# Kernel optimization log

Measured on AMD Instinct MI355X. Metric: run time of the kernel, lower is better.

Reference implementation:

```python
import jax, jax.numpy as jnp
import numpy as np

B, NQ, NKV = 2, 1024, 4096
DQ = 1024          # query_dim == context_dim
H, DH = 16, 64     # heads, dim_head
INNER = H * DH     # 1024
SCALE = DH ** -0.5


def setup_inputs() -> dict:
    key = jax.random.key(0)
    ks = jax.random.split(key, 6)
    s = 1.0 / np.sqrt(DQ)
    return {
        "x": jax.random.normal(ks[0], (B, NQ, DQ), dtype=jnp.float32),
        "context": jax.random.normal(ks[1], (B, NKV, DQ), dtype=jnp.float32),
        "Wq": jax.random.normal(ks[2], (DQ, INNER), dtype=jnp.float32) * s,
        "Wkv": jax.random.normal(ks[3], (DQ, 2 * INNER), dtype=jnp.float32) * s,
        "Wout": jax.random.normal(ks[4], (INNER, DQ), dtype=jnp.float32) * (1.0 / np.sqrt(INNER)),
        "b_out": jax.random.normal(ks[5], (DQ,), dtype=jnp.float32) * 0.01,
    }


def _split_heads(t):
    # b n (h d) -> b h n d
    b, n, _ = t.shape
    return t.reshape(b, n, H, DH).transpose(0, 2, 1, 3)


def reference(x, context, Wq, Wkv, Wout, b_out):
    q = x @ Wq                       # [B, NQ, INNER]
    kv = context @ Wkv               # [B, NKV, 2*INNER]
    k, v = jnp.split(kv, 2, axis=-1)
    q, k, v = map(_split_heads, (q, k, v))          # [B, H, n, DH]
    sim = jnp.einsum("bhid,bhjd->bhij", q, k) * SCALE  # [B, H, NQ, NKV]
    attn = jax.nn.softmax(sim, axis=-1)
    out = jnp.einsum("bhij,bhjd->bhid", attn, v)       # [B, H, NQ, DH]
    out = out.transpose(0, 2, 1, 3).reshape(B, NQ, INNER)  # (b h) n d -> b n (h d)
    return out @ Wout + b_out
```

## Files before the change

### kernel.cpp

```cpp
#include <hip/hip_runtime.h>
#include <stdint.h>

#define B_    2
#define NQ_   1024
#define NKV_  4096
#define DQ_   1024
#define H_    16
#define DH_   64
#define INNER_ 1024

typedef unsigned short u16;
typedef uint32_t u32;
typedef __bf16 bf16x8 __attribute__((ext_vector_type(8)));
typedef float  f32x4  __attribute__((ext_vector_type(4)));

__device__ __forceinline__ u16 f2bf(float x) {
  union { float f; uint32_t u; } v; v.f = x;
  uint32_t r = v.u + 0x7FFFu + ((v.u >> 16) & 1u);
  return (u16)(r >> 16);
}
__device__ __forceinline__ u32 pack2(float a, float b) {
  return (u32)f2bf(a) | ((u32)f2bf(b) << 16);
}
__device__ __forceinline__ u32 pack2rn(float a, float b) {
  union { float f; u32 u; } x, y; x.f = a; y.f = b;
  return __builtin_amdgcn_perm(y.u + 0x8000u, x.u + 0x8000u, 0x07060302u);
}
__device__ __forceinline__ float bf2f(u16 s) {
  union { float f; uint32_t u; } v; v.u = ((uint32_t)s) << 16; return v.f;
}

__device__ __forceinline__ void gload16(const void* g, void* l) {
  __builtin_amdgcn_global_load_lds((const __attribute__((address_space(1))) void*)g,
                                   (__attribute__((address_space(3))) void*)l,
                                   16, 0, 0);
}

__global__ __launch_bounds__(256) void prep(const float* __restrict__ x,
                                            const float* __restrict__ ctx,
                                            const float* __restrict__ Wq,
                                            const float* __restrict__ Wkv,
                                            const float* __restrict__ Wout,
                                            u16* __restrict__ xb,
                                            u16* __restrict__ ctxb,
                                            u16* __restrict__ WqT,
                                            u16* __restrict__ WkvT,
                                            u16* __restrict__ WoutT) {
  int bid = blockIdx.x;
  if (bid < 10240) {
    const float* src; u16* dst; int blk;
    if (bid < 2048) { src = x; dst = xb; blk = bid; }
    else            { src = ctx; dst = ctxb; blk = bid - 2048; }
    int i = (blk * 256 + threadIdx.x) * 4;
    float4 v = *(const float4*)(src + i);
    uint2 o; o.x = pack2(v.x, v.y); o.y = pack2(v.z, v.w);
    *(uint2*)(dst + i) = o;
    return;
  }
  __shared__ float tile[32][33];
  const float* W; u16* Wt; int K, N, local, nsh;
  if (bid < 11264)      { W = Wq;   Wt = WqT;   K = 1024; N = 1024; local = bid - 10240; nsh = 5; }
  else if (bid < 13312) { W = Wkv;  Wt = WkvT;  K = 1024; N = 2048; local = bid - 11264; nsh = 6; }
  else                  { W = Wout; Wt = WoutT; K = 1024; N = 1024; local = bid - 13312; nsh = 5; }
  int n0 = (local & ((1 << nsh) - 1)) * 32;
  int k0 = (local >> nsh) * 32;
  int tx = threadIdx.x & 31, ty = threadIdx.x >> 5;
  for (int i = ty; i < 32; i += 8)
    tile[i][tx] = W[(size_t)(k0 + i) * N + n0 + tx];
  __syncthreads();
  for (int i = ty; i < 32; i += 8)
    Wt[(size_t)(n0 + i) * K + k0 + tx] = f2bf(tile[tx][i]);
}

__global__ __launch_bounds__(256) void qkv_gemm(const u16* __restrict__ xb,
                                                const u16* __restrict__ ctxb,
                                                const u16* __restrict__ WqT,
                                                const u16* __restrict__ WkvT,
                                                u16* __restrict__ qb,
                                                u16* __restrict__ kb,
                                                u16* __restrict__ vTb) {
  __shared__ __align__(16) u16 As[128 * 32];
  __shared__ __align__(16) u16 Bs[128 * 32];
  const int tid = threadIdx.x;
  const int lane = tid & 63;
  const int w = tid >> 6;
  const int wr = w >> 1, wc = w & 1;
  const int l15 = lane & 15, quad = lane >> 4;

  int bid = blockIdx.x;
  const u16 *A, *Bt; int m0, n0, mode;
  if (bid < 128) { m0 = (bid >> 3) * 128; n0 = (bid & 7) * 128; A = xb;   Bt = WqT;  mode = 0; }
  else { bid -= 128; m0 = (bid >> 4) * 128; n0 = (bid & 15) * 128; A = ctxb; Bt = WkvT;
         mode = (n0 < 1024) ? 1 : 2; }
  const int K = 1024;

  const u16* Ab = A + (size_t)m0 * K;
  const u16* Bb = Bt + (size_t)n0 * K;

  f32x4 acc[4][4] = {};

  const int q1 = w * 64 + lane;
  const int q2 = q1 + 256;
  const int ar1 = q1 >> 2, ac1 = (q1 & 3) << 3;
  const int ar2 = q2 >> 2, ac2 = (q2 & 3) << 3;

  for (int k0 = 0; k0 < K; k0 += 32) {
    __syncthreads();
    gload16(Ab + (size_t)ar1 * K + k0 + ac1, &As[w * 512]);
    gload16(Ab + (size_t)ar2 * K + k0 + ac2, &As[2048 + w * 512]);
    gload16(Bb + (size_t)ar1 * K + k0 + ac1, &Bs[w * 512]);
    gload16(Bb + (size_t)ar2 * K + k0 + ac2, &Bs[2048 + w * 512]);
    __syncthreads();
    bf16x8 af[4], bfr[4];
#pragma unroll
    for (int i = 0; i < 4; ++i)
      af[i] = *(const bf16x8*)&As[(wr * 64 + i * 16 + l15) * 32 + quad * 8];
#pragma unroll
    for (int j = 0; j < 4; ++j)
      bfr[j] = *(const bf16x8*)&Bs[(wc * 64 + j * 16 + l15) * 32 + quad * 8];
#pragma unroll
    for (int i = 0; i < 4; ++i)
#pragma unroll
      for (int j = 0; j < 4; ++j)
        acc[i][j] = __builtin_amdgcn_mfma_f32_16x16x32_bf16(af[i], bfr[j], acc[i][j], 0, 0, 0);
  }

  if (mode == 2) {
    const int bb = m0 >> 12;
#pragma unroll
    for (int i = 0; i < 4; ++i) {
      int kvr = (m0 & 4095) + wr * 64 + i * 16 + quad * 4;
#pragma unroll
      for (int j = 0; j < 4; ++j) {
        int c = (n0 - 1024) + wc * 64 + j * 16 + l15;
        int h = c >> 6, dh = c & 63;
        uint2 st;
        st.x = pack2(acc[i][j][0], acc[i][j][1]);
        st.y = pack2(acc[i][j][2], acc[i][j][3]);
        *(uint2*)&vTb[((size_t)((bb * 16 + h) * 64 + dh)) * NKV_ + kvr] = st;
      }
    }
    return;
  }

  u16* out = (mode == 0) ? qb : kb;
  const int N = 1024;
#pragma unroll
  for (int i = 0; i < 4; ++i)
#pragma unroll
    for (int j = 0; j < 4; ++j) {
      int col = n0 + wc * 64 + j * 16 + l15;
#pragma unroll
      for (int r = 0; r < 4; ++r) {
        int row = m0 + wr * 64 + i * 16 + quad * 4 + r;
        out[(size_t)row * N + col] = f2bf(acc[i][j][r]);
      }
    }
}

__global__ __launch_bounds__(256) void out_gemm(const u16* __restrict__ A,
                                                const u16* __restrict__ Bt,
                                                float* __restrict__ Cout,
                                                const float* __restrict__ bias) {
  __shared__ __align__(16) u16 As[128 * 32];
  __shared__ __align__(16) u16 Bs[128 * 32];
  const int tid = threadIdx.x;
  const int lane = tid & 63;
  const int w = tid >> 6;
  const int wr = w >> 1, wc = w & 1;
  const int l15 = lane & 15, quad = lane >> 4;
  const int m0 = blockIdx.y * 128, n0 = blockIdx.x * 128;
  const int K = 1024, N = 1024;

  const u16* Ab = A + (size_t)m0 * K;
  const u16* Bb = Bt + (size_t)n0 * K;
  f32x4 acc[4][4] = {};

  const int q1 = w * 64 + lane, q2 = q1 + 256;
  const int ar1 = q1 >> 2, ac1 = (q1 & 3) << 3;
  const int ar2 = q2 >> 2, ac2 = (q2 & 3) << 3;

  for (int k0 = 0; k0 < K; k0 += 32) {
    __syncthreads();
    gload16(Ab + (size_t)ar1 * K + k0 + ac1, &As[w * 512]);
    gload16(Ab + (size_t)ar2 * K + k0 + ac2, &As[2048 + w * 512]);
    gload16(Bb + (size_t)ar1 * K + k0 + ac1, &Bs[w * 512]);
    gload16(Bb + (size_t)ar2 * K + k0 + ac2, &Bs[2048 + w * 512]);
    __syncthreads();
    bf16x8 af[4], bfr[4];
#pragma unroll
    for (int i = 0; i < 4; ++i)
      af[i] = *(const bf16x8*)&As[(wr * 64 + i * 16 + l15) * 32 + quad * 8];
#pragma unroll
    for (int j = 0; j < 4; ++j)
      bfr[j] = *(const bf16x8*)&Bs[(wc * 64 + j * 16 + l15) * 32 + quad * 8];
#pragma unroll
    for (int i = 0; i < 4; ++i)
#pragma unroll
      for (int j = 0; j < 4; ++j)
        acc[i][j] = __builtin_amdgcn_mfma_f32_16x16x32_bf16(af[i], bfr[j], acc[i][j], 0, 0, 0);
  }

#pragma unroll
  for (int i = 0; i < 4; ++i)
#pragma unroll
    for (int j = 0; j < 4; ++j) {
      int col = n0 + wc * 64 + j * 16 + l15;
      float bv = bias[col];
#pragma unroll
      for (int r = 0; r < 4; ++r) {
        int row = m0 + wr * 64 + i * 16 + quad * 4 + r;
        Cout[(size_t)row * N + col] = acc[i][j][r] + bv;
      }
    }
}

__global__ __launch_bounds__(256, 2) void attn_kernel(const u16* __restrict__ qg,
                                                      const u16* __restrict__ kb,
                                                      const u16* __restrict__ vT,
                                                      u16* __restrict__ attn_out) {
  __shared__ __align__(16) u16 Ks[128 * 64];
  __shared__ __align__(16) u16 Vs[64 * 128];
  __shared__ __align__(16) u32 P32[4 * 4 * 16 * 20];
  __shared__ float Lr[4][4][16];

  const int tid = threadIdx.x;
  const int lane = tid & 63;
  const int w = tid >> 6;
  const int l15 = lane & 15, quad = lane >> 4;
  const int bh = blockIdx.x, b = bh >> 4, h = bh & 15;
  const int q0 = blockIdx.y * 64;

  const float SC = 0.125f * 1.44269504088896340736f;
  union { u16 s[8]; bf16x8 v; } qf[4][2];
#pragma unroll
  for (int t = 0; t < 4; ++t)
#pragma unroll
    for (int kc = 0; kc < 2; ++kc) {
      const u16* qp = qg + (size_t)(b * NQ_ + q0 + t * 16 + l15) * INNER_ + h * 64 +
                      kc * 32 + quad * 8;
      union { u16 s[8]; uint4 u; } tmp;
      tmp.u = *(const uint4*)qp;
#pragma unroll
      for (int e = 0; e < 8; ++e) qf[t][kc].s[e] = f2bf(bf2f(tmp.s[e]) * SC);
    }

  f32x4 Oacc[4][4] = {};
  float l_lane[4] = {0.f, 0.f, 0.f, 0.f};

  for (int it = 0; it < 32; ++it) {
    const int j0 = it * 128;
    __syncthreads();
#pragma unroll
    for (int i = 0; i < 4; ++i) {
      int s = i * 256 + tid;
      int kr = s >> 3, kg = (s ^ kr) & 7;
      gload16(kb + (size_t)(b * NKV_ + j0 + kr) * 1024 + h * 64 + kg * 8,
              &Ks[(i * 256 + w * 64) * 8]);
      int vr = s >> 4, vg = (s ^ vr) & 15;
      gload16(vT + (size_t)(bh * 64 + vr) * NKV_ + j0 + vg * 8,
              &Vs[(i * 256 + w * 64) * 8]);
    }
    __syncthreads();

    bf16x8 kf[2][2];
#pragma unroll
    for (int kvt = 0; kvt < 2; ++kvt)
#pragma unroll
      for (int kc = 0; kc < 2; ++kc)
        kf[kvt][kc] = *(const bf16x8*)
          &Ks[(w * 32 + kvt * 16 + l15) * 64 + (((kc * 4 + quad) ^ l15) & 7) * 8];
    f32x4 sacc[2][4] = {};
#pragma unroll
    for (int kvt = 0; kvt < 2; ++kvt)
#pragma unroll
      for (int t = 0; t < 4; ++t)
#pragma unroll
        for (int kc = 0; kc < 2; ++kc)
          sacc[kvt][t] = __builtin_amdgcn_mfma_f32_16x16x32_bf16(
              kf[kvt][kc], qf[t][kc].v, sacc[kvt][t], 0, 0, 0);

#pragma unroll
    for (int kvt = 0; kvt < 2; ++kvt)
#pragma unroll
      for (int t = 0; t < 4; ++t) {
        float p0 = __builtin_amdgcn_exp2f(sacc[kvt][t][0]);
        float p1 = __builtin_amdgcn_exp2f(sacc[kvt][t][1]);
        float p2 = __builtin_amdgcn_exp2f(sacc[kvt][t][2]);
        float p3 = __builtin_amdgcn_exp2f(sacc[kvt][t][3]);
        l_lane[t] += (p0 + p1) + (p2 + p3);
        uint2 pk; pk.x = pack2rn(p0, p1); pk.y = pack2rn(p2, p3);
        *(uint2*)&P32[((w * 4 + t) * 16 + l15) * 20 + kvt * 8 + quad * 2] = pk;
      }

    bf16x8 vf[4], pf[4];
#pragma unroll
    for (int d = 0; d < 4; ++d)
      vf[d] = *(const bf16x8*)
        &Vs[(d * 16 + l15) * 128 + (((w * 4 + quad) ^ l15) & 15) * 8];
#pragma unroll
    for (int t = 0; t < 4; ++t)
      pf[t] = *(const bf16x8*)&P32[((w * 4 + t) * 16 + l15) * 20 + quad * 4];
#pragma unroll
    for (int d = 0; d < 4; ++d)
#pragma unroll
      for (int t = 0; t < 4; ++t)
        Oacc[d][t] = __builtin_amdgcn_mfma_f32_16x16x32_bf16(vf[d], pf[t], Oacc[d][t],
                                                             0, 0, 0);
  }

#pragma unroll
  for (int t = 0; t < 4; ++t) {
    l_lane[t] += __shfl_xor(l_lane[t], 16);
    l_lane[t] += __shfl_xor(l_lane[t], 32);
  }
  if (quad == 0) {
#pragma unroll
    for (int t = 0; t < 4; ++t) Lr[w][t][l15] = l_lane[t];
  }
  __syncthreads();
  float inv = 1.0f / (Lr[0][w][l15] + Lr[1][w][l15] + Lr[2][w][l15] + Lr[3][w][l15]);

  float* red = (float*)P32;
  u16* ob = attn_out + (size_t)(b * NQ_ + q0 + w * 16 + l15) * INNER_ + h * 64;
#pragma unroll
  for (int d = 0; d < 4; ++d) {
    __syncthreads();
#pragma unroll
    for (int t = 0; t < 4; ++t)
      *(f32x4*)&red[(w * 4 + t) * 256 + quad * 64 + l15 * 4] = Oacc[d][t];
    __syncthreads();
    f32x4 r = *(const f32x4*)&red[(0 * 4 + w) * 256 + quad * 64 + l15 * 4];
#pragma unroll
    for (int ww = 1; ww < 4; ++ww) {
      f32x4 c = *(const f32x4*)&red[(ww * 4 + w) * 256 + quad * 64 + l15 * 4];
      r[0] += c[0]; r[1] += c[1]; r[2] += c[2]; r[3] += c[3];
    }
    *(u32*)(ob + d * 16 + quad * 4)     = pack2(r[0] * inv, r[1] * inv);
    *(u32*)(ob + d * 16 + quad * 4 + 2) = pack2(r[2] * inv, r[3] * inv);
  }
}

extern "C" void kernel_launch(void* const* d_in, const int* in_sizes, int n_in,
                              void* d_out, int out_size, void* d_ws, size_t ws_size,
                              hipStream_t stream) {
  const float* x    = (const float*)d_in[0];
  const float* ctx  = (const float*)d_in[1];
  const float* Wq   = (const float*)d_in[2];
  const float* Wkv  = (const float*)d_in[3];
  const float* Wout = (const float*)d_in[4];
  const float* bout = (const float*)d_in[5];

  char* ws = (char*)d_ws;
  u16* xb    = (u16*)(ws + (size_t)( 0u << 20));
  u16* ab    = (u16*)(ws + (size_t)( 0u << 20));
  u16* ctxb  = (u16*)(ws + (size_t)( 4u << 20));
  u16* WqT   = (u16*)(ws + (size_t)(20u << 20));
  u16* WkvT  = (u16*)(ws + (size_t)(22u << 20));
  u16* WoutT = (u16*)(ws + (size_t)(26u << 20));
  u16* qb    = (u16*)(ws + (size_t)(28u << 20));
  u16* kb    = (u16*)(ws + (size_t)(32u << 20));
  u16* vTb   = (u16*)(ws + (size_t)(48u << 20));

  prep<<<14336, 256, 0, stream>>>(x, ctx, Wq, Wkv, Wout, xb, ctxb, WqT, WkvT, WoutT);
  qkv_gemm<<<1152, 256, 0, stream>>>(xb, ctxb, WqT, WkvT, qb, kb, vTb);
  attn_kernel<<<dim3(32, 16), 256, 0, stream>>>(qb, kb, vTb, ab);
  out_gemm<<<dim3(8, 16), 256, 0, stream>>>(ab, WoutT, (float*)d_out, bout);
}
```

Measured before the change: 231.1 us.

## Fuse fp32-to-bf16 activation conversion into QKV GEMM and shrink out_gemm tiles

Removes the separate pass that converts x and context to bf16. The QKV GEMM now loads fp32 activations straight into LDS with an XOR-swizzled layout and converts them to bf16 while building MFMA fragments. This saves a full write and re-read of the bf16 activation copies, in exchange for twice the LDS traffic on the A operand and extra pack instructions in the inner loop. Separately, out_gemm switches to 64x128 tiles, giving 256 blocks instead of 128 so more CUs are busy.

```diff
diff --git a/kernel.cpp b/kernel.cpp
--- a/kernel.cpp
+++ b/kernel.cpp
@@ -36,32 +36,18 @@
                                    16, 0, 0);
 }
 
-__global__ __launch_bounds__(256) void prep(const float* __restrict__ x,
-                                            const float* __restrict__ ctx,
-                                            const float* __restrict__ Wq,
+__global__ __launch_bounds__(256) void prep(const float* __restrict__ Wq,
                                             const float* __restrict__ Wkv,
                                             const float* __restrict__ Wout,
-                                            u16* __restrict__ xb,
-                                            u16* __restrict__ ctxb,
                                             u16* __restrict__ WqT,
                                             u16* __restrict__ WkvT,
                                             u16* __restrict__ WoutT) {
-  int bid = blockIdx.x;
-  if (bid < 10240) {
-    const float* src; u16* dst; int blk;
-    if (bid < 2048) { src = x; dst = xb; blk = bid; }
-    else            { src = ctx; dst = ctxb; blk = bid - 2048; }
-    int i = (blk * 256 + threadIdx.x) * 4;
-    float4 v = *(const float4*)(src + i);
-    uint2 o; o.x = pack2(v.x, v.y); o.y = pack2(v.z, v.w);
-    *(uint2*)(dst + i) = o;
-    return;
-  }
   __shared__ float tile[32][33];
+  int u = blockIdx.x;
   const float* W; u16* Wt; int K, N, local, nsh;
-  if (bid < 11264)      { W = Wq;   Wt = WqT;   K = 1024; N = 1024; local = bid - 10240; nsh = 5; }
-  else if (bid < 13312) { W = Wkv;  Wt = WkvT;  K = 1024; N = 2048; local = bid - 11264; nsh = 6; }
-  else                  { W = Wout; Wt = WoutT; K = 1024; N = 1024; local = bid - 13312; nsh = 5; }
+  if (u < 1024)      { W = Wq;   Wt = WqT;   K = 1024; N = 1024; local = u;        nsh = 5; }
+  else if (u < 3072) { W = Wkv;  Wt = WkvT;  K = 1024; N = 2048; local = u - 1024; nsh = 6; }
+  else               { W = Wout; Wt = WoutT; K = 1024; N = 1024; local = u - 3072; nsh = 5; }
   int n0 = (local & ((1 << nsh) - 1)) * 32;
   int k0 = (local >> nsh) * 32;
   int tx = threadIdx.x & 31, ty = threadIdx.x >> 5;
@@ -72,15 +58,15 @@
     Wt[(size_t)(n0 + i) * K + k0 + tx] = f2bf(tile[tx][i]);
 }
 
-__global__ __launch_bounds__(256) void qkv_gemm(const u16* __restrict__ xb,
-                                                const u16* __restrict__ ctxb,
+__global__ __launch_bounds__(256) void qkv_gemm(const float* __restrict__ x,
+                                                const float* __restrict__ ctx,
                                                 const u16* __restrict__ WqT,
                                                 const u16* __restrict__ WkvT,
                                                 u16* __restrict__ qb,
                                                 u16* __restrict__ kb,
                                                 u16* __restrict__ vTb) {
-  __shared__ __align__(16) u16 As[128 * 32];
-  __shared__ __align__(16) u16 Bs[128 * 32];
+  __shared__ __align__(16) float Afs[128 * 32];
+  __shared__ __align__(16) u16  Bs[128 * 32];
   const int tid = threadIdx.x;
   const int lane = tid & 63;
   const int w = tid >> 6;
@@ -88,33 +74,48 @@
   const int l15 = lane & 15, quad = lane >> 4;
 
   int bid = blockIdx.x;
-  const u16 *A, *Bt; int m0, n0, mode;
-  if (bid < 128) { m0 = (bid >> 3) * 128; n0 = (bid & 7) * 128; A = xb;   Bt = WqT;  mode = 0; }
-  else { bid -= 128; m0 = (bid >> 4) * 128; n0 = (bid & 15) * 128; A = ctxb; Bt = WkvT;
+  const float* A; const u16* Bt; int m0, n0, mode;
+  if (bid < 128) { m0 = (bid >> 3) * 128; n0 = (bid & 7) * 128; A = x;   Bt = WqT;  mode = 0; }
+  else { bid -= 128; m0 = (bid >> 4) * 128; n0 = (bid & 15) * 128; A = ctx; Bt = WkvT;
          mode = (n0 < 1024) ? 1 : 2; }
   const int K = 1024;
 
-  const u16* Ab = A + (size_t)m0 * K;
+  const float* Ab = A + (size_t)m0 * K;
   const u16* Bb = Bt + (size_t)n0 * K;
 
   f32x4 acc[4][4] = {};
 
-  const int q1 = w * 64 + lane;
-  const int q2 = q1 + 256;
-  const int ar1 = q1 >> 2, ac1 = (q1 & 3) << 3;
-  const int ar2 = q2 >> 2, ac2 = (q2 & 3) << 3;
+  const int q1 = w * 64 + lane, q2 = q1 + 256;
+  const int br1 = q1 >> 2, bc1 = (q1 & 3) << 3;
+  const int br2 = q2 >> 2, bc2 = (q2 & 3) << 3;
+  int arow[4], ag[4];
+#pragma unroll
+  for (int j = 0; j < 4; ++j) {
+    int s = j * 256 + tid;
+    arow[j] = s >> 3;
+    ag[j] = (s ^ arow[j]) & 7;
+  }
 
   for (int k0 = 0; k0 < K; k0 += 32) {
     __syncthreads();
-    gload16(Ab + (size_t)ar1 * K + k0 + ac1, &As[w * 512]);
-    gload16(Ab + (size_t)ar2 * K + k0 + ac2, &As[2048 + w * 512]);
-    gload16(Bb + (size_t)ar1 * K + k0 + ac1, &Bs[w * 512]);
-    gload16(Bb + (size_t)ar2 * K + k0 + ac2, &Bs[2048 + w * 512]);
+#pragma unroll
+    for (int j = 0; j < 4; ++j)
+      gload16(Ab + (size_t)arow[j] * K + k0 + ag[j] * 4, &Afs[(j * 256 + w * 64) * 4]);
+    gload16(Bb + (size_t)br1 * K + k0 + bc1, &Bs[w * 512]);
+    gload16(Bb + (size_t)br2 * K + k0 + bc2, &Bs[2048 + w * 512]);
     __syncthreads();
     bf16x8 af[4], bfr[4];
 #pragma unroll
-    for (int i = 0; i < 4; ++i)
-      af[i] = *(const bf16x8*)&As[(wr * 64 + i * 16 + l15) * 32 + quad * 8];
+    for (int i = 0; i < 4; ++i) {
+      int r = wr * 64 + i * 16 + l15;
+      int g0 = (2 * quad) ^ (r & 7), g1 = (2 * quad + 1) ^ (r & 7);
+      f32x4 a0 = *(const f32x4*)&Afs[r * 32 + g0 * 4];
+      f32x4 a1 = *(const f32x4*)&Afs[r * 32 + g1 * 4];
+      union { u32 u[4]; bf16x8 v; } cv;
+      cv.u[0] = pack2rn(a0[0], a0[1]); cv.u[1] = pack2rn(a0[2], a0[3]);
+      cv.u[2] = pack2rn(a1[0], a1[1]); cv.u[3] = pack2rn(a1[2], a1[3]);
+      af[i] = cv.v;
+    }
 #pragma unroll
     for (int j = 0; j < 4; ++j)
       bfr[j] = *(const bf16x8*)&Bs[(wc * 64 + j * 16 + l15) * 32 + quad * 8];
@@ -162,54 +163,55 @@
                                                 const u16* __restrict__ Bt,
                                                 float* __restrict__ Cout,
                                                 const float* __restrict__ bias) {
-  __shared__ __align__(16) u16 As[128 * 32];
+  __shared__ __align__(16) u16 As[64 * 32];
   __shared__ __align__(16) u16 Bs[128 * 32];
   const int tid = threadIdx.x;
   const int lane = tid & 63;
   const int w = tid >> 6;
   const int wr = w >> 1, wc = w & 1;
   const int l15 = lane & 15, quad = lane >> 4;
-  const int m0 = blockIdx.y * 128, n0 = blockIdx.x * 128;
+  const int unit = blockIdx.x;
+  const int m0 = (unit >> 3) * 64, n0 = (unit & 7) * 128;
   const int K = 1024, N = 1024;
 
   const u16* Ab = A + (size_t)m0 * K;
   const u16* Bb = Bt + (size_t)n0 * K;
-  f32x4 acc[4][4] = {};
-
+  f32x4 acc[2][4] = {};
+
+  const int ar = tid >> 2, ac = (tid & 3) << 3;
   const int q1 = w * 64 + lane, q2 = q1 + 256;
-  const int ar1 = q1 >> 2, ac1 = (q1 & 3) << 3;
-  const int ar2 = q2 >> 2, ac2 = (q2 & 3) << 3;
+  const int br1 = q1 >> 2, bc1 = (q1 & 3) << 3;
+  const int br2 = q2 >> 2, bc2 = (q2 & 3) << 3;
 
   for (int k0 = 0; k0 < K; k0 += 32) {
     __syncthreads();
-    gload16(Ab + (size_t)ar1 * K + k0 + ac1, &As[w * 512]);
-    gload16(Ab + (size_t)ar2 * K + k0 + ac2, &As[2048 + w * 512]);
-    gload16(Bb + (size_t)ar1 * K + k0 + ac1, &Bs[w * 512]);
-    gload16(Bb + (size_t)ar2 * K + k0 + ac2, &Bs[2048 + w * 512]);
-    __syncthreads();
-    bf16x8 af[4], bfr[4];
-#pragma unroll
-    for (int i = 0; i < 4; ++i)
-      af[i] = *(const bf16x8*)&As[(wr * 64 + i * 16 + l15) * 32 + quad * 8];
+    gload16(Ab + (size_t)ar * K + k0 + ac, &As[w * 512]);
+    gload16(Bb + (size_t)br1 * K + k0 + bc1, &Bs[w * 512]);
+    gload16(Bb + (size_t)br2 * K + k0 + bc2, &Bs[2048 + w * 512]);
+    __syncthreads();
+    bf16x8 af[2], bfr[4];
+#pragma unroll
+    for (int i = 0; i < 2; ++i)
+      af[i] = *(const bf16x8*)&As[(wr * 32 + i * 16 + l15) * 32 + quad * 8];
 #pragma unroll
     for (int j = 0; j < 4; ++j)
       bfr[j] = *(const bf16x8*)&Bs[(wc * 64 + j * 16 + l15) * 32 + quad * 8];
 #pragma unroll
-    for (int i = 0; i < 4; ++i)
+    for (int i = 0; i < 2; ++i)
 #pragma unroll
       for (int j = 0; j < 4; ++j)
         acc[i][j] = __builtin_amdgcn_mfma_f32_16x16x32_bf16(af[i], bfr[j], acc[i][j], 0, 0, 0);
   }
 
 #pragma unroll
-  for (int i = 0; i < 4; ++i)
+  for (int i = 0; i < 2; ++i)
 #pragma unroll
     for (int j = 0; j < 4; ++j) {
       int col = n0 + wc * 64 + j * 16 + l15;
       float bv = bias[col];
 #pragma unroll
       for (int r = 0; r < 4; ++r) {
-        int row = m0 + wr * 64 + i * 16 + quad * 4 + r;
+        int row = m0 + wr * 32 + i * 16 + quad * 4 + r;
         Cout[(size_t)row * N + col] = acc[i][j][r] + bv;
       }
     }
@@ -352,9 +354,7 @@
   const float* bout = (const float*)d_in[5];
 
   char* ws = (char*)d_ws;
-  u16* xb    = (u16*)(ws + (size_t)( 0u << 20));
   u16* ab    = (u16*)(ws + (size_t)( 0u << 20));
-  u16* ctxb  = (u16*)(ws + (size_t)( 4u << 20));
   u16* WqT   = (u16*)(ws + (size_t)(20u << 20));
   u16* WkvT  = (u16*)(ws + (size_t)(22u << 20));
   u16* WoutT = (u16*)(ws + (size_t)(26u << 20));
@@ -362,8 +362,8 @@
   u16* kb    = (u16*)(ws + (size_t)(32u << 20));
   u16* vTb   = (u16*)(ws + (size_t)(48u << 20));
 
-  prep<<<14336, 256, 0, stream>>>(x, ctx, Wq, Wkv, Wout, xb, ctxb, WqT, WkvT, WoutT);
-  qkv_gemm<<<1152, 256, 0, stream>>>(xb, ctxb, WqT, WkvT, qb, kb, vTb);
+  prep<<<4096, 256, 0, stream>>>(Wq, Wkv, Wout, WqT, WkvT, WoutT);
+  qkv_gemm<<<1152, 256, 0, stream>>>(x, ctx, WqT, WkvT, qb, kb, vTb);
   attn_kernel<<<dim3(32, 16), 256, 0, stream>>>(qb, kb, vTb, ab);
-  out_gemm<<<dim3(8, 16), 256, 0, stream>>>(ab, WoutT, (float*)d_out, bout);
-}
+  out_gemm<<<256, 256, 0, stream>>>(ab, WoutT, (float*)d_out, bout);
+}
```

Measured after the change: 249.3 us. 7.9% more time.

## Make QKV GEMM persistent with atomic tile queue and halve out GEMM M-tile

Applied to the files above, without the earlier changes.

The QKV projection GEMM becomes a persistent kernel of 512 blocks that fetch further 128x128 tiles from a global atomic counter. The counter is reset in the prep kernel and placed in the output buffer. The output projection GEMM switches to 64x128 tiles, doubling its block count to 256 to fill more compute units. This aims to reduce tail imbalance and launch granularity, at the cost of atomic traffic and lower per-block reuse in the output GEMM.

```diff
diff --git a/kernel.cpp b/kernel.cpp
--- a/kernel.cpp
+++ b/kernel.cpp
@@ -45,8 +45,10 @@
                                             u16* __restrict__ ctxb,
                                             u16* __restrict__ WqT,
                                             u16* __restrict__ WkvT,
-                                            u16* __restrict__ WoutT) {
+                                            u16* __restrict__ WoutT,
+                                            u32* __restrict__ cnt) {
   int bid = blockIdx.x;
+  if (bid == 0 && threadIdx.x == 0) *cnt = 0u;
   if (bid < 10240) {
     const float* src; u16* dst; int blk;
     if (bid < 2048) { src = x; dst = xb; blk = bid; }
@@ -72,22 +74,19 @@
     Wt[(size_t)(n0 + i) * K + k0 + tx] = f2bf(tile[tx][i]);
 }
 
-__global__ __launch_bounds__(256) void qkv_gemm(const u16* __restrict__ xb,
-                                                const u16* __restrict__ ctxb,
-                                                const u16* __restrict__ WqT,
-                                                const u16* __restrict__ WkvT,
-                                                u16* __restrict__ qb,
-                                                u16* __restrict__ kb,
-                                                u16* __restrict__ vTb) {
-  __shared__ __align__(16) u16 As[128 * 32];
-  __shared__ __align__(16) u16 Bs[128 * 32];
-  const int tid = threadIdx.x;
+__device__ __forceinline__ void qkv_tile(int unit, int tid, u16* As, u16* Bs,
+                                         const u16* __restrict__ xb,
+                                         const u16* __restrict__ ctxb,
+                                         const u16* __restrict__ WqT,
+                                         const u16* __restrict__ WkvT,
+                                         u16* __restrict__ qb, u16* __restrict__ kb,
+                                         u16* __restrict__ vTb) {
   const int lane = tid & 63;
   const int w = tid >> 6;
   const int wr = w >> 1, wc = w & 1;
   const int l15 = lane & 15, quad = lane >> 4;
 
-  int bid = blockIdx.x;
+  int bid = unit;
   const u16 *A, *Bt; int m0, n0, mode;
   if (bid < 128) { m0 = (bid >> 3) * 128; n0 = (bid & 7) * 128; A = xb;   Bt = WqT;  mode = 0; }
   else { bid -= 128; m0 = (bid >> 4) * 128; n0 = (bid & 15) * 128; A = ctxb; Bt = WkvT;
@@ -158,58 +157,80 @@
     }
 }
 
+__global__ __launch_bounds__(256) void qkv_gemm(const u16* __restrict__ xb,
+                                                const u16* __restrict__ ctxb,
+                                                const u16* __restrict__ WqT,
+                                                const u16* __restrict__ WkvT,
+                                                u16* __restrict__ qb,
+                                                u16* __restrict__ kb,
+                                                u16* __restrict__ vTb,
+                                                u32* __restrict__ cnt) {
+  __shared__ __align__(16) u16 As[128 * 32];
+  __shared__ __align__(16) u16 Bs[128 * 32];
+  __shared__ int sh_next;
+  const int tid = threadIdx.x;
+  int unit = blockIdx.x;
+  while (unit < 1152) {
+    qkv_tile(unit, tid, As, Bs, xb, ctxb, WqT, WkvT, qb, kb, vTb);
+    if (tid == 0) sh_next = 512 + (int)atomicAdd(cnt, 1u);
+    __syncthreads();
+    unit = sh_next;
+  }
+}
+
 __global__ __launch_bounds__(256) void out_gemm(const u16* __restrict__ A,
                                                 const u16* __restrict__ Bt,
                                                 float* __restrict__ Cout,
                                                 const float* __restrict__ bias) {
-  __shared__ __align__(16) u16 As[128 * 32];
+  __shared__ __align__(16) u16 As[64 * 32];
   __shared__ __align__(16) u16 Bs[128 * 32];
   const int tid = threadIdx.x;
   const int lane = tid & 63;
   const int w = tid >> 6;
   const int wr = w >> 1, wc = w & 1;
   const int l15 = lane & 15, quad = lane >> 4;
-  const int m0 = blockIdx.y * 128, n0 = blockIdx.x * 128;
+  const int unit = blockIdx.x;
+  const int m0 = (unit >> 3) * 64, n0 = (unit & 7) * 128;
   const int K = 1024, N = 1024;
 
   const u16* Ab = A + (size_t)m0 * K;
   const u16* Bb = Bt + (size_t)n0 * K;
-  f32x4 acc[4][4] = {};
-
+  f32x4 acc[2][4] = {};
+
+  const int ar = tid >> 2, ac = (tid & 3) << 3;
   const int q1 = w * 64 + lane, q2 = q1 + 256;
-  const int ar1 = q1 >> 2, ac1 = (q1 & 3) << 3;
-  const int ar2 = q2 >> 2, ac2 = (q2 & 3) << 3;
+  const int br1 = q1 >> 2, bc1 = (q1 & 3) << 3;
+  const int br2 = q2 >> 2, bc2 = (q2 & 3) << 3;
 
   for (int k0 = 0; k0 < K; k0 += 32) {
     __syncthreads();
-    gload16(Ab + (size_t)ar1 * K + k0 + ac1, &As[w * 512]);
-    gload16(Ab + (size_t)ar2 * K + k0 + ac2, &As[2048 + w * 512]);
-    gload16(Bb + (size_t)ar1 * K + k0 + ac1, &Bs[w * 512]);
-    gload16(Bb + (size_t)ar2 * K + k0 + ac2, &Bs[2048 + w * 512]);
-    __syncthreads();
-    bf16x8 af[4], bfr[4];
-#pragma unroll
-    for (int i = 0; i < 4; ++i)
-      af[i] = *(const bf16x8*)&As[(wr * 64 + i * 16 + l15) * 32 + quad * 8];
+    gload16(Ab + (size_t)ar * K + k0 + ac, &As[w * 512]);
+    gload16(Bb + (size_t)br1 * K + k0 + bc1, &Bs[w * 512]);
+    gload16(Bb + (size_t)br2 * K + k0 + bc2, &Bs[2048 + w * 512]);
+    __syncthreads();
+    bf16x8 af[2], bfr[4];
+#pragma unroll
+    for (int i = 0; i < 2; ++i)
+      af[i] = *(const bf16x8*)&As[(wr * 32 + i * 16 + l15) * 32 + quad * 8];
 #pragma unroll
     for (int j = 0; j < 4; ++j)
       bfr[j] = *(const bf16x8*)&Bs[(wc * 64 + j * 16 + l15) * 32 + quad * 8];
 #pragma unroll
-    for (int i = 0; i < 4; ++i)
+    for (int i = 0; i < 2; ++i)
 #pragma unroll
       for (int j = 0; j < 4; ++j)
         acc[i][j] = __builtin_amdgcn_mfma_f32_16x16x32_bf16(af[i], bfr[j], acc[i][j], 0, 0, 0);
   }
 
 #pragma unroll
-  for (int i = 0; i < 4; ++i)
+  for (int i = 0; i < 2; ++i)
 #pragma unroll
     for (int j = 0; j < 4; ++j) {
       int col = n0 + wc * 64 + j * 16 + l15;
       float bv = bias[col];
 #pragma unroll
       for (int r = 0; r < 4; ++r) {
-        int row = m0 + wr * 64 + i * 16 + quad * 4 + r;
+        int row = m0 + wr * 32 + i * 16 + quad * 4 + r;
         Cout[(size_t)row * N + col] = acc[i][j][r] + bv;
       }
     }
@@ -361,9 +382,10 @@
   u16* qb    = (u16*)(ws + (size_t)(28u << 20));
   u16* kb    = (u16*)(ws + (size_t)(32u << 20));
   u16* vTb   = (u16*)(ws + (size_t)(48u << 20));
-
-  prep<<<14336, 256, 0, stream>>>(x, ctx, Wq, Wkv, Wout, xb, ctxb, WqT, WkvT, WoutT);
-  qkv_gemm<<<1152, 256, 0, stream>>>(xb, ctxb, WqT, WkvT, qb, kb, vTb);
+  u32* cnt   = (u32*)d_out;
+
+  prep<<<14336, 256, 0, stream>>>(x, ctx, Wq, Wkv, Wout, xb, ctxb, WqT, WkvT, WoutT, cnt);
+  qkv_gemm<<<512, 256, 0, stream>>>(xb, ctxb, WqT, WkvT, qb, kb, vTb, cnt);
   attn_kernel<<<dim3(32, 16), 256, 0, stream>>>(qb, kb, vTb, ab);
-  out_gemm<<<dim3(8, 16), 256, 0, stream>>>(ab, WoutT, (float*)d_out, bout);
-}
+  out_gemm<<<256, 256, 0, stream>>>(ab, WoutT, (float*)d_out, bout);
+}
```

New measurement: 240.5 us. +4.1%, slower.
